# Kernel optimization log

Hardware: AMD Instinct MI355X
Metric: run time of the kernel (lower is better)

The kernel has to match this reference:

```python
import jax, jax.numpy as jnp
import numpy as np

INPUT_SIZE = 34
HIDDEN = 4
NUM_CLASSES = 3
B, T = 4096, 200


def setup_inputs() -> dict:
    key = jax.random.key(0)
    ks = jax.random.split(key, 8)
    k = 1.0 / np.sqrt(HIDDEN)  # torch default uniform init bound
    u = lambda kk, shape: jax.random.uniform(kk, shape, jnp.float32, -k, k)
    x = jax.random.normal(ks[0], (B, T, INPUT_SIZE), jnp.float32)
    W_ih = u(ks[1], (4 * HIDDEN, INPUT_SIZE))   # gate order: i, f, g, o
    W_hh = u(ks[2], (4 * HIDDEN, HIDDEN))
    b_ih = u(ks[3], (4 * HIDDEN,))
    b_hh = u(ks[4], (4 * HIDDEN,))
    W_fc = u(ks[5], (NUM_CLASSES, HIDDEN))
    b_fc = u(ks[6], (NUM_CLASSES,))
    return {"x": x, "W_ih": W_ih, "W_hh": W_hh, "b_ih": b_ih,
            "b_hh": b_hh, "W_fc": W_fc, "b_fc": b_fc}


def reference(x, W_ih, W_hh, b_ih, b_hh, W_fc, b_fc):
    Bsz = x.shape[0]
    H = W_hh.shape[1]
    # Precompute input contributions for all timesteps: [B, T, 4H]
    x_gates = jnp.einsum('btd,gd->btg', x, W_ih) + b_ih + b_hh
    x_gates = jnp.swapaxes(x_gates, 0, 1)  # [T, B, 4H] for scan

    def step(carry, xg_t):
        h, c = carry
        gates = xg_t + h @ W_hh.T          # [B, 4H]
        i, f, g, o = jnp.split(gates, 4, axis=-1)
        i = jax.nn.sigmoid(i)
        f = jax.nn.sigmoid(f)
        g = jnp.tanh(g)
        o = jax.nn.sigmoid(o)
        c = f * c + i * g
        h = o * jnp.tanh(c)
        return (h, c), None

    h0 = jnp.zeros((Bsz, H), x.dtype)
    c0 = jnp.zeros((Bsz, H), x.dtype)
    (h_last, _), _ = jax.lax.scan(step, (h0, c0), x_gates)
    # dropout is identity in eval mode
    return h_last @ W_fc.T + b_fc  # [B, num_classes]
```

## Files before the change

kernel.cpp:

```cpp
#include <hip/hip_runtime.h>

#define B_SZ 4096
#define T_SZ 200
#define IN_SZ 34

__device__ __forceinline__ float sigf(float x) {
    return 1.0f / (1.0f + __expf(-x));
}
__device__ __forceinline__ float tanh_f(float x) {
    return 2.0f / (1.0f + __expf(-2.0f * x)) - 1.0f;
}

__device__ __forceinline__ float quad_bcast0(float v) {
    int s = __float_as_int(v);
    return __int_as_float(__builtin_amdgcn_update_dpp(s, s, 0x00, 0xf, 0xf, true));
}
__device__ __forceinline__ float quad_bcast1(float v) {
    int s = __float_as_int(v);
    return __int_as_float(__builtin_amdgcn_update_dpp(s, s, 0x55, 0xf, 0xf, true));
}
__device__ __forceinline__ float quad_bcast2(float v) {
    int s = __float_as_int(v);
    return __int_as_float(__builtin_amdgcn_update_dpp(s, s, 0xAA, 0xf, 0xf, true));
}
__device__ __forceinline__ float quad_bcast3(float v) {
    int s = __float_as_int(v);
    return __int_as_float(__builtin_amdgcn_update_dpp(s, s, 0xFF, 0xf, 0xf, true));
}

__global__ __launch_bounds__(256) void xgates_kernel(
    const float* __restrict__ x, const float* __restrict__ W_ih,
    const float* __restrict__ b_ih, const float* __restrict__ b_hh,
    float* __restrict__ xg) {
  int row = blockIdx.x * 256 + threadIdx.x;
  float xr[IN_SZ];
  const float2* xp = reinterpret_cast<const float2*>(x + (size_t)row * IN_SZ);
  #pragma unroll
  for (int k = 0; k < IN_SZ / 2; ++k) {
    float2 v = xp[k];
    xr[2 * k] = v.x;
    xr[2 * k + 1] = v.y;
  }
  float acc[16];
  #pragma unroll
  for (int g = 0; g < 16; ++g) acc[g] = b_ih[g] + b_hh[g];
  #pragma unroll
  for (int k = 0; k < IN_SZ; ++k) {
    #pragma unroll
    for (int g = 0; g < 16; ++g)
      acc[g] = fmaf(xr[k], W_ih[g * IN_SZ + k], acc[g]);
  }
  float4* op = reinterpret_cast<float4*>(xg + (size_t)row * 16);
  #pragma unroll
  for (int j = 0; j < 4; ++j)
    op[j] = make_float4(acc[j], acc[4 + j], acc[8 + j], acc[12 + j]);
}

#define U_SZ 10
__global__ __launch_bounds__(64) void lstm_scan(
    const float* __restrict__ xg, const float* __restrict__ W_hh,
    const float* __restrict__ W_fc, const float* __restrict__ b_fc,
    float* __restrict__ out) {
  int tid = blockIdx.x * 64 + threadIdx.x;
  int b = tid >> 2;
  int j = tid & 3;
  float Wi[4], Wf[4], Wg[4], Wo[4];
  #pragma unroll
  for (int k = 0; k < 4; ++k) {
    Wi[k] = W_hh[(0 + j) * 4 + k];
    Wf[k] = W_hh[(4 + j) * 4 + k];
    Wg[k] = W_hh[(8 + j) * 4 + k];
    Wo[k] = W_hh[(12 + j) * 4 + k];
  }
  float h[4] = {0.f, 0.f, 0.f, 0.f};
  float c = 0.f;

  auto step = [&](float4 g4) {
    float pi = g4.x, pf = g4.y, pg = g4.z, po = g4.w;
    #pragma unroll
    for (int k = 0; k < 4; ++k) {
      pi = fmaf(Wi[k], h[k], pi);
      pf = fmaf(Wf[k], h[k], pf);
      pg = fmaf(Wg[k], h[k], pg);
      po = fmaf(Wo[k], h[k], po);
    }
    float iv = sigf(pi);
    float fv = sigf(pf);
    float gv = tanh_f(pg);
    float ov = sigf(po);
    c = fmaf(fv, c, iv * gv);
    float hj = ov * tanh_f(c);
    h[0] = quad_bcast0(hj);
    h[1] = quad_bcast1(hj);
    h[2] = quad_bcast2(hj);
    h[3] = quad_bcast3(hj);
  };

  const float4* xp = reinterpret_cast<const float4*>(xg) + (size_t)b * (T_SZ * 4) + j;
  float4 bufA[U_SZ], bufB[U_SZ];
  #pragma unroll
  for (int u = 0; u < U_SZ; ++u) bufA[u] = xp[4 * u];

  #pragma unroll 1
  for (int blk = 0; blk < 20; blk += 2) {
    const float4* p1 = xp + (size_t)(blk + 1) * (4 * U_SZ);
    #pragma unroll
    for (int u = 0; u < U_SZ; ++u) bufB[u] = p1[4 * u];
    #pragma unroll
    for (int u = 0; u < U_SZ; ++u) step(bufA[u]);
    if (blk + 2 < 20) {
      const float4* p2 = xp + (size_t)(blk + 2) * (4 * U_SZ);
      #pragma unroll
      for (int u = 0; u < U_SZ; ++u) bufA[u] = p2[4 * u];
    }
    #pragma unroll
    for (int u = 0; u < U_SZ; ++u) step(bufB[u]);
  }

  if (j < 3) {
    float acc = b_fc[j];
    #pragma unroll
    for (int k = 0; k < 4; ++k) acc = fmaf(W_fc[j * 4 + k], h[k], acc);
    out[b * 3 + j] = acc;
  }
}

__global__ __launch_bounds__(256) void lstm_fused(
    const float* __restrict__ x, const float* __restrict__ W_ih,
    const float* __restrict__ W_hh, const float* __restrict__ b_ih,
    const float* __restrict__ b_hh, const float* __restrict__ W_fc,
    const float* __restrict__ b_fc, float* __restrict__ out) {
  __shared__ float Ws[16 * IN_SZ];
  for (int i = threadIdx.x; i < 16 * IN_SZ; i += 256) Ws[i] = W_ih[i];
  __syncthreads();
  int tid = blockIdx.x * 256 + threadIdx.x;
  int b = tid >> 2;
  int j = tid & 3;
  float bi = b_ih[0 + j] + b_hh[0 + j];
  float bf = b_ih[4 + j] + b_hh[4 + j];
  float bg = b_ih[8 + j] + b_hh[8 + j];
  float bo = b_ih[12 + j] + b_hh[12 + j];
  float Wi[4], Wf[4], Wg[4], Wo[4];
  #pragma unroll
  for (int k = 0; k < 4; ++k) {
    Wi[k] = W_hh[(0 + j) * 4 + k];
    Wf[k] = W_hh[(4 + j) * 4 + k];
    Wg[k] = W_hh[(8 + j) * 4 + k];
    Wo[k] = W_hh[(12 + j) * 4 + k];
  }
  float h[4] = {0.f, 0.f, 0.f, 0.f};
  float c = 0.f;
  const float2* xp = reinterpret_cast<const float2*>(x + (size_t)b * T_SZ * IN_SZ);
  int lbase = (threadIdx.x & 63) & ~3;
  for (int t = 0; t < T_SZ; ++t) {
    float xr[IN_SZ];
    #pragma unroll
    for (int k = 0; k < IN_SZ / 2; ++k) {
      float2 v = xp[(size_t)t * (IN_SZ / 2) + k];
      xr[2 * k] = v.x;
      xr[2 * k + 1] = v.y;
    }
    float pi = bi, pf = bf, pg = bg, po = bo;
    #pragma unroll
    for (int k = 0; k < IN_SZ; ++k) {
      pi = fmaf(xr[k], Ws[(0 + j) * IN_SZ + k], pi);
      pf = fmaf(xr[k], Ws[(4 + j) * IN_SZ + k], pf);
      pg = fmaf(xr[k], Ws[(8 + j) * IN_SZ + k], pg);
      po = fmaf(xr[k], Ws[(12 + j) * IN_SZ + k], po);
    }
    #pragma unroll
    for (int k = 0; k < 4; ++k) {
      pi = fmaf(Wi[k], h[k], pi);
      pf = fmaf(Wf[k], h[k], pf);
      pg = fmaf(Wg[k], h[k], pg);
      po = fmaf(Wo[k], h[k], po);
    }
    float iv = sigf(pi);
    float fv = sigf(pf);
    float gv = tanh_f(pg);
    float ov = sigf(po);
    c = fmaf(fv, c, iv * gv);
    float hj = ov * tanh_f(c);
    h[0] = __shfl(hj, lbase + 0);
    h[1] = __shfl(hj, lbase + 1);
    h[2] = __shfl(hj, lbase + 2);
    h[3] = __shfl(hj, lbase + 3);
  }
  if (j < 3) {
    float acc = b_fc[j];
    #pragma unroll
    for (int k = 0; k < 4; ++k) acc = fmaf(W_fc[j * 4 + k], h[k], acc);
    out[b * 3 + j] = acc;
  }
}

extern "C" void kernel_launch(void* const* d_in, const int* in_sizes, int n_in,
                              void* d_out, int out_size, void* d_ws, size_t ws_size,
                              hipStream_t stream) {
  const float* x    = (const float*)d_in[0];
  const float* W_ih = (const float*)d_in[1];
  const float* W_hh = (const float*)d_in[2];
  const float* b_ih = (const float*)d_in[3];
  const float* b_hh = (const float*)d_in[4];
  const float* W_fc = (const float*)d_in[5];
  const float* b_fc = (const float*)d_in[6];
  float* out = (float*)d_out;

  const size_t need = (size_t)B_SZ * T_SZ * 16 * sizeof(float);
  if (ws_size >= need) {
    float* xg = (float*)d_ws;
    hipLaunchKernelGGL(xgates_kernel, dim3(B_SZ * T_SZ / 256), dim3(256), 0, stream,
                       x, W_ih, b_ih, b_hh, xg);
    hipLaunchKernelGGL(lstm_scan, dim3(B_SZ * 4 / 64), dim3(64), 0, stream,
                       xg, W_hh, W_fc, b_fc, out);
  } else {
    hipLaunchKernelGGL(lstm_fused, dim3(B_SZ * 4 / 256), dim3(256), 0, stream,
                       x, W_ih, W_hh, b_ih, b_hh, W_fc, b_fc, out);
  }
}
```

Before: 89.69 us.

## Split xgates row dot-products across 16 lanes with DPP quad reductions

Rewrites the input-gate projection kernel so that 16 lanes cooperate on each (b,t) row instead of one thread per row. Each lane keeps a 4x10 slice of W_ih in registers, loads a contiguous 32-byte chunk of the row, and combines partial sums with DPP quad reductions. The grid becomes a fixed 2048 persistent-style blocks that each loop over their rows. The intent is to coalesce the x reads, which were strided per thread before, and to cut per-thread register and weight-load pressure. In exchange it adds cross-lane reduction work, and only one lane in four does the stores.

```diff
diff --git a/kernel.cpp b/kernel.cpp
--- a/kernel.cpp
+++ b/kernel.cpp
@@ -3,6 +3,9 @@
 #define B_SZ 4096
 #define T_SZ 200
 #define IN_SZ 34
+#define XG_BLOCKS 2048
+#define ROWS_PER_BLOCK (B_SZ * T_SZ / XG_BLOCKS)
+#define XG_ITERS (ROWS_PER_BLOCK / 16)
 
 __device__ __forceinline__ float sigf(float x) {
     return 1.0f / (1.0f + __expf(-x));
@@ -26,34 +29,72 @@
 __device__ __forceinline__ float quad_bcast3(float v) {
     int s = __float_as_int(v);
     return __int_as_float(__builtin_amdgcn_update_dpp(s, s, 0xFF, 0xf, 0xf, true));
+}
+__device__ __forceinline__ float quad_red(float v) {
+    int s = __float_as_int(v);
+    v += __int_as_float(__builtin_amdgcn_update_dpp(s, s, 0xB1, 0xf, 0xf, true));
+    s = __float_as_int(v);
+    v += __int_as_float(__builtin_amdgcn_update_dpp(s, s, 0x4E, 0xf, 0xf, true));
+    return v;
 }
 
 __global__ __launch_bounds__(256) void xgates_kernel(
     const float* __restrict__ x, const float* __restrict__ W_ih,
     const float* __restrict__ b_ih, const float* __restrict__ b_hh,
     float* __restrict__ xg) {
-  int row = blockIdx.x * 256 + threadIdx.x;
-  float xr[IN_SZ];
-  const float2* xp = reinterpret_cast<const float2*>(x + (size_t)row * IN_SZ);
-  #pragma unroll
-  for (int k = 0; k < IN_SZ / 2; ++k) {
-    float2 v = xp[k];
-    xr[2 * k] = v.x;
-    xr[2 * k + 1] = v.y;
-  }
-  float acc[16];
-  #pragma unroll
-  for (int g = 0; g < 16; ++g) acc[g] = b_ih[g] + b_hh[g];
-  #pragma unroll
-  for (int k = 0; k < IN_SZ; ++k) {
-    #pragma unroll
-    for (int g = 0; g < 16; ++g)
-      acc[g] = fmaf(xr[k], W_ih[g * IN_SZ + k], acc[g]);
-  }
-  float4* op = reinterpret_cast<float4*>(xg + (size_t)row * 16);
-  #pragma unroll
-  for (int j = 0; j < 4; ++j)
-    op[j] = make_float4(acc[j], acc[4 + j], acc[8 + j], acc[12 + j]);
+  const int tid = threadIdx.x;
+  const int lane16 = tid & 15;
+  const int q = lane16 >> 2;
+  const int r = lane16 & 3;
+  const int slot = tid >> 4;
+
+  float wv[4][10];
+  #pragma unroll
+  for (int z = 0; z < 4; ++z) {
+    #pragma unroll
+    for (int kk = 0; kk < 8; ++kk)
+      wv[z][kk] = W_ih[(z * 4 + q) * IN_SZ + r * 8 + kk];
+    wv[z][8] = (r == 0) ? W_ih[(z * 4 + q) * IN_SZ + 32] : 0.f;
+    wv[z][9] = (r == 0) ? W_ih[(z * 4 + q) * IN_SZ + 33] : 0.f;
+  }
+  float bias[4];
+  #pragma unroll
+  for (int z = 0; z < 4; ++z) bias[z] = b_ih[z * 4 + q] + b_hh[z * 4 + q];
+
+  const size_t row0 = (size_t)blockIdx.x * ROWS_PER_BLOCK + slot;
+  #pragma unroll 1
+  for (int i = 0; i < XG_ITERS; ++i) {
+    size_t row = row0 + (size_t)i * 16;
+    const char* rp = reinterpret_cast<const char*>(x) + row * 136;
+    float xv[10];
+    #pragma unroll
+    for (int m = 0; m < 4; ++m) {
+      float2 v = *reinterpret_cast<const float2*>(rp + r * 32 + m * 8);
+      xv[2 * m] = v.x;
+      xv[2 * m + 1] = v.y;
+    }
+    if (r == 0) {
+      float2 vt = *reinterpret_cast<const float2*>(rp + 128);
+      xv[8] = vt.x;
+      xv[9] = vt.y;
+    } else {
+      xv[8] = 0.f;
+      xv[9] = 0.f;
+    }
+    float acc[4];
+    #pragma unroll
+    for (int z = 0; z < 4; ++z) {
+      float a = 0.f;
+      #pragma unroll
+      for (int kk = 0; kk < 10; ++kk) a = fmaf(xv[kk], wv[z][kk], a);
+      acc[z] = quad_red(a);
+    }
+    if (r == 0) {
+      float4 o = make_float4(acc[0] + bias[0], acc[1] + bias[1],
+                             acc[2] + bias[2], acc[3] + bias[3]);
+      *reinterpret_cast<float4*>(xg + row * 16 + q * 4) = o;
+    }
+  }
 }
 
 #define U_SZ 10
@@ -209,7 +250,7 @@
   const size_t need = (size_t)B_SZ * T_SZ * 16 * sizeof(float);
   if (ws_size >= need) {
     float* xg = (float*)d_ws;
-    hipLaunchKernelGGL(xgates_kernel, dim3(B_SZ * T_SZ / 256), dim3(256), 0, stream,
+    hipLaunchKernelGGL(xgates_kernel, dim3(XG_BLOCKS), dim3(256), 0, stream,
                        x, W_ih, b_ih, b_hh, xg);
     hipLaunchKernelGGL(lstm_scan, dim3(B_SZ * 4 / 64), dim3(64), 0, stream,
                        xg, W_hh, W_fc, b_fc, out);
```

Result: no change. 90.17 us (+0.5%).
